# Optimization experiments

Measured on AMD Instinct MI355X. Metric: run time of the kernel, lower is better.

Reference implementation:

```python
import jax, jax.numpy as jnp
import numpy as np

N_SAMPLES = 512
N_SKIP = 10      # __init__ N: number of skipped steps between kept samples
BURNIN = 100


def _perm_weight(bigram, start, end, p):
    # bigram[p[:-1], p[1:]].sum() + start[p[0]] + end[p[-1]]
    return bigram[p[:-1], p[1:]].sum() + start[p[0]] + end[p[-1]]


def setup_inputs() -> dict:
    key = jax.random.key(0)
    k1, k2, k3 = jax.random.split(key, 3)
    n_words = 4096
    return {
        "n_words": n_words,
        "bigram": jax.random.normal(k1, (n_words, n_words), dtype=jnp.float32),
        "start": jax.random.normal(k2, (n_words,), dtype=jnp.float32),
        "end": jax.random.normal(k3, (n_words,), dtype=jnp.float32),
    }


def reference(n_words, bigram, start, end):
    # Total chain length: burn-in, then one kept sample every (N_SKIP+1) steps.
    T = BURNIN + (N_SAMPLES - 1) * (N_SKIP + 1) + 1
    key = jax.random.key(42)
    kinit, kchain = jax.random.split(key)

    permut0 = jax.random.permutation(kinit, n_words).astype(jnp.int32)
    w0 = _perm_weight(bigram, start, end, permut0)
    idx = jnp.arange(n_words, dtype=jnp.int32)

    def step(carry, k):
        permut, w = carry
        kl, ka, kr, ku = jax.random.split(k, 4)
        # segment length l in [1, n_words-1], start a in [0, n_words-l]
        l = jax.random.randint(kl, (), 1, n_words)
        a = jax.random.randint(ka, (), 0, n_words - l + 1)
        b = a + l
        r = jax.random.randint(kr, (), 0, n_words - l)  # [0, n_words-l-1]
        c = (b + r + 1) % (n_words + 1)
        # The 2-opt block move is a cyclic rotation of one contiguous span:
        #   a < c : rotate span [a, c) left-shifting the block [a,b) after [b,c)
        #   a >= c: rotate span [c, b) moving block [a,b) before [c,a)
        lo = jnp.where(a < c, a, c).astype(jnp.int32)
        hi = jnp.where(a < c, c, b).astype(jnp.int32)
        shift = jnp.where(a < c, b - a, a - c).astype(jnp.int32)
        span = hi - lo  # always >= 1
        src = jnp.where((idx >= lo) & (idx < hi),
                        lo + (idx - lo + shift) % span,
                        idx)
        permut2 = permut[src]
        w2 = _perm_weight(bigram, start, end, permut2)
        u = jax.random.uniform(ku, ())
        # accept iff min(1, exp(w2-w)) > u  <=>  min(w2-w, 0) > log(u)
        accept = jnp.minimum(w2 - w, jnp.float32(0.0)) > jnp.log(u)
        permut_n = jnp.where(accept, permut2, permut)
        w_n = jnp.where(accept, w2, w)
        return (permut_n, w_n), permut_n

    keys = jax.random.split(kchain, T)
    _, perms = jax.lax.scan(step, (permut0, w0), keys)  # [T, n_words]
    samples = perms[BURNIN::(N_SKIP + 1)][:N_SAMPLES]   # [n_samples, n_words]
    return samples
```

## Files before the change

kernel.cpp:

```cpp
#include <hip/hip_runtime.h>
#include <stdint.h>
#include <math.h>

#define NW      4096
#define TSTEPS  5722
#define BURN    100
#define SSTRIDE 11
#define NTHR    256
#define NBOUND  522

struct K2 { uint32_t a, b; };

__device__ __forceinline__ K2 tf(uint32_t k0, uint32_t k1, uint32_t c0, uint32_t c1) {
  uint32_t ks2 = k0 ^ k1 ^ 0x1BD11BDAu;
  uint32_t x0 = c0 + k0, x1 = c1 + k1;
#define RR(r) { x0 += x1; x1 = (x1 << (r)) | (x1 >> (32 - (r))); x1 ^= x0; }
  RR(13) RR(15) RR(26) RR(6)
  x0 += k1;  x1 += ks2 + 1u;
  RR(17) RR(29) RR(16) RR(24)
  x0 += ks2; x1 += k0 + 2u;
  RR(13) RR(15) RR(26) RR(6)
  x0 += k0;  x1 += k1 + 3u;
  RR(17) RR(29) RR(16) RR(24)
  x0 += k1;  x1 += ks2 + 4u;
  RR(13) RR(15) RR(26) RR(6)
  x0 += ks2; x1 += k0 + 5u;
#undef RR
  K2 r; r.a = x0; r.b = x1; return r;
}

__device__ __forceinline__ uint32_t xbits(K2 k) {
  K2 r = tf(k.a, k.b, 0u, 0u);
  return r.a ^ r.b;
}

__device__ __forceinline__ uint32_t ri_off(K2 key, uint32_t span) {
  K2 k1 = tf(key.a, key.b, 0u, 0u);
  K2 k2 = tf(key.a, key.b, 0u, 1u);
  uint32_t hb = xbits(k1);
  uint32_t lb = xbits(k2);
  uint32_t m = 65536u % span;
  m = (m * m) % span;
  return ((hb % span) * m + (lb % span)) % span;
}

__device__ __noinline__ void make_prop(uint32_t kca, uint32_t kcb, int t,
                                       uint32_t& lohi, uint32_t& shv, float& lg) {
  K2 kt = tf(kca, kcb, 0u, (uint32_t)t);
  K2 kl = tf(kt.a, kt.b, 0u, 0u);
  K2 ka = tf(kt.a, kt.b, 0u, 1u);
  K2 kr = tf(kt.a, kt.b, 0u, 2u);
  K2 ku = tf(kt.a, kt.b, 0u, 3u);
  uint32_t l = 1u + ri_off(kl, 4095u);
  uint32_t a = ri_off(ka, 4097u - l);
  uint32_t b = a + l;
  uint32_t r = ri_off(kr, 4096u - l);
  uint32_t c = (b + r + 1u) % 4097u;
  uint32_t lo, hi, sh;
  if (a < c) { lo = a; hi = c; sh = b - a; }
  else       { lo = c; hi = b; sh = a - c; }
  uint32_t ub = xbits(ku);
  float uf = __uint_as_float((ub >> 9) | 0x3F800000u) - 1.0f;
  lohi = lo | (hi << 16);
  shv  = sh;
  lg   = (float)log((double)uf);
}

__device__ __forceinline__ uint32_t smap2(uint32_t i, uint32_t lo, uint32_t span, uint32_t sh) {
  uint32_t t = i - lo;
  uint32_t u = t + sh;
  u = (u >= span) ? u - span : u;
  return (t < span) ? lo + u : i;
}

__global__ void prop_kernel(uint4* __restrict__ gprop) {
  int t = blockIdx.x * 256 + threadIdx.x;
  if (t >= TSTEPS) return;
  K2 kchain = tf(0u, 42u, 0u, 1u);
  uint32_t lohi, shv; float lg;
  make_prop(kchain.a, kchain.b, t, lohi, shv, lg);
  gprop[t] = make_uint4(lohi, shv, __float_as_uint(lg), 0u);
}

#define SYNC() do { asm volatile("s_waitcnt lgkmcnt(0)" ::: "memory"); \
                    __builtin_amdgcn_s_barrier(); } while (0)

template<int CTRL>
__device__ __forceinline__ double dpp_f64(double v) {
  long long s = __double_as_longlong(v);
  int lo = (int)(s & 0xFFFFFFFFll);
  int hi = (int)(s >> 32);
  lo = __builtin_amdgcn_update_dpp(0, lo, CTRL, 0xF, 0xF, true);
  hi = __builtin_amdgcn_update_dpp(0, hi, CTRL, 0xF, 0xF, true);
  return __longlong_as_double((long long)(unsigned)lo | ((long long)hi << 32));
}

__device__ __forceinline__ uint32_t compose_sw(uint32_t pos, int jc,
                                               const uint32_t (&mlh)[12],
                                               const uint32_t (&msh)[12]) {
  switch (jc) {
    case 11: pos = smap2(pos, mlh[10] & 0xFFFFu, mlh[10] >> 16, msh[10]); [[fallthrough]];
    case 10: pos = smap2(pos, mlh[9]  & 0xFFFFu, mlh[9]  >> 16, msh[9]);  [[fallthrough]];
    case 9:  pos = smap2(pos, mlh[8]  & 0xFFFFu, mlh[8]  >> 16, msh[8]);  [[fallthrough]];
    case 8:  pos = smap2(pos, mlh[7]  & 0xFFFFu, mlh[7]  >> 16, msh[7]);  [[fallthrough]];
    case 7:  pos = smap2(pos, mlh[6]  & 0xFFFFu, mlh[6]  >> 16, msh[6]);  [[fallthrough]];
    case 6:  pos = smap2(pos, mlh[5]  & 0xFFFFu, mlh[5]  >> 16, msh[5]);  [[fallthrough]];
    case 5:  pos = smap2(pos, mlh[4]  & 0xFFFFu, mlh[4]  >> 16, msh[4]);  [[fallthrough]];
    case 4:  pos = smap2(pos, mlh[3]  & 0xFFFFu, mlh[3]  >> 16, msh[3]);  [[fallthrough]];
    case 3:  pos = smap2(pos, mlh[2]  & 0xFFFFu, mlh[2]  >> 16, msh[2]);  [[fallthrough]];
    case 2:  pos = smap2(pos, mlh[1]  & 0xFFFFu, mlh[1]  >> 16, msh[1]);  [[fallthrough]];
    case 1:  pos = smap2(pos, mlh[0]  & 0xFFFFu, mlh[0]  >> 16, msh[0]);  break;
    default: break;
  }
  return pos;
}

__device__ __forceinline__ void mat_emit(int tid, int jcu, uint32_t cur,
                                         const uint32_t* __restrict__ s_mvlh,
                                         const uint32_t* __restrict__ s_mvsh,
                                         uint32_t (*s_base)[NW],
                                         bool emit, int row, int* __restrict__ out) {
  uint32_t posa[16];
  #pragma unroll
  for (int k = 0; k < 16; ++k) posa[k] = (uint32_t)tid + (uint32_t)k * 256u;
  for (int j = jcu - 1; j >= 0; --j) {
    uint32_t lh = s_mvlh[j], sh = s_mvsh[j];
    uint32_t lo = lh & 0xFFFFu, sp = lh >> 16;
    #pragma unroll
    for (int k = 0; k < 16; ++k) posa[k] = smap2(posa[k], lo, sp, sh);
  }
  uint32_t vals[16];
  #pragma unroll
  for (int k = 0; k < 16; ++k) vals[k] = s_base[cur][posa[k]];
  #pragma unroll
  for (int k = 0; k < 16; ++k) {
    uint32_t i = (uint32_t)tid + (uint32_t)k * 256u;
    s_base[cur ^ 1u][i] = vals[k];
    if (emit) out[(size_t)row * NW + i] = (int)vals[k];
  }
}

__device__ __forceinline__ void stepf(
    int T, uint32_t lane, float sgn, float& ld, bool& accp, int& jc,
    uint32_t (&mlh)[12], uint32_t (&msh)[12],
    uint32_t& s0lh, uint32_t& s0sh, float& s0lg,
    uint32_t& s1lh, uint32_t& s1sh, float& s1lg,
    uint32_t& s2lh, uint32_t& s2sh, float& s2lg,
    uint32_t& s3lh, uint32_t& s3sh, float& s3lg,
    const uint32_t* __restrict__ sbase,
    uint32_t* __restrict__ s_mvlh, uint32_t* __restrict__ s_mvsh,
    const float* __restrict__ bigram, const float* __restrict__ startw,
    const float* __restrict__ endw, const uint4* __restrict__ gprop,
    uint32_t kca, uint32_t kcb) {

  uint32_t p    = lane & 7u;
  uint32_t vset = (lane >> 3) & 3u;

  uint32_t lo2 = s2lh & 0xFFFFu, hi2 = s2lh >> 16, sh2 = s2sh;
  uint32_t g0 = lo2, g1 = lo2 + sh2, g2v = g1 - 1u, g3 = hi2 - 1u;
  uint32_t g4 = (lo2 > 0u) ? lo2 - 1u : 0u;
  uint32_t g5 = (hi2 < (uint32_t)NW) ? hi2 : 0u;
  uint32_t pos = (p == 0u) ? g0 : (p == 1u) ? g1 : (p == 2u) ? g2v
               : (p == 3u) ? g3 : (p == 4u) ? g4 : g5;

  uint32_t lo1 = s1lh & 0xFFFFu, sp1 = (s1lh >> 16) - lo1, sh1 = s1sh;
  uint32_t lo0 = s0lh & 0xFFFFu, sp0 = (s0lh >> 16) - lo0, sh0 = s0sh;
  if (vset & 1u) pos = smap2(pos, lo1, sp1, sh1);
  if (vset & 2u) pos = smap2(pos, lo0, sp0, sh0);
  pos = compose_sw(pos, jc, mlh, msh);
  uint32_t val = sbase[pos];

  int tq = T + 4; if (tq > TSTEPS - 1) tq = TSTEPS - 1;
  uint32_t nlh, nsh; float nlg;
  if (gprop) { uint4 gp = gprop[tq]; nlh = gp.x; nsh = gp.y; nlg = __uint_as_float(gp.z); }
  else       { make_prop(kca, kcb, tq, nlh, nsh, nlg); }

  double du = (double)(ld * sgn);
  du += dpp_f64<0x111>(du);
  du += dpp_f64<0x112>(du);
  du += dpp_f64<0x114>(du);
  double dmin = du < 0.0 ? du : 0.0;
  int accl = (dmin > (double)s0lg) ? 1 : 0;
  int accR = __builtin_amdgcn_readlane(accl, 7);
  int accA = __builtin_amdgcn_readlane(accl, 15);
  int acc = accp ? accA : accR;

  uint32_t qv = (uint32_t)__shfl((int)val, (int)((uint32_t)acc * 16u + lane), 64);
  uint32_t base8 = lane & ~7u;
  uint32_t rsrc = (p == 0u) ? 3u : (p == 1u) ? 2u : (p <= 3u) ? 4u : (p == 4u) ? 2u : 3u;
  uint32_t csrc = (p == 0u) ? 0u : (p <= 2u) ? 1u : (p == 3u) ? 0u : 5u;
  uint32_t row = (uint32_t)__shfl((int)qv, (int)(base8 + rsrc), 64);
  uint32_t col = (uint32_t)__shfl((int)qv, (int)(base8 + csrc), 64);
  bool isbi = (p < 2u) || ((p < 4u) ? (lo2 > 0u) : (hi2 < (uint32_t)NW));
  const float* addr = isbi ? (bigram + (size_t)row * NW + col)
                           : ((p < 4u) ? (startw + col) : (endw + row));
  bool isload = (vset < 2u) && (p < 6u);
  if (isload) ld = *addr;

  if (acc) {
    uint32_t nv = lo0 | (sp0 << 16);
    switch (jc) {
      case 0:  mlh[0]  = nv; msh[0]  = sh0; break;
      case 1:  mlh[1]  = nv; msh[1]  = sh0; break;
      case 2:  mlh[2]  = nv; msh[2]  = sh0; break;
      case 3:  mlh[3]  = nv; msh[3]  = sh0; break;
      case 4:  mlh[4]  = nv; msh[4]  = sh0; break;
      case 5:  mlh[5]  = nv; msh[5]  = sh0; break;
      case 6:  mlh[6]  = nv; msh[6]  = sh0; break;
      case 7:  mlh[7]  = nv; msh[7]  = sh0; break;
      case 8:  mlh[8]  = nv; msh[8]  = sh0; break;
      case 9:  mlh[9]  = nv; msh[9]  = sh0; break;
      case 10: mlh[10] = nv; msh[10] = sh0; break;
      default: break;
    }
    if (lane == 0u) { s_mvlh[jc] = nv; s_mvsh[jc] = sh0; }
    jc++;
  }
  accp = (acc != 0);

  s0lh = s1lh; s0sh = s1sh; s0lg = s1lg;
  s1lh = s2lh; s1sh = s2sh; s1lg = s2lg;
  s2lh = s3lh; s2sh = s3sh; s2lg = s3lg;
  s3lh = nlh;  s3sh = nsh;  s3lg = nlg;
}

__global__ __launch_bounds__(NTHR)
void TwoOptMCMC_86148454023515_kernel(const float* __restrict__ bigram,
                                      const float* __restrict__ startw,
                                      const float* __restrict__ endw,
                                      int* __restrict__ out,
                                      const uint4* __restrict__ gprop) {
  __shared__ __align__(16) uint32_t s_base[2][NW];
  __shared__ uint32_t s_mvlh[12];
  __shared__ uint32_t s_mvsh[12];
  __shared__ uint32_t s_jc[1];

  unsigned long long* s_comp = (unsigned long long*)s_base;
  const int tid = threadIdx.x;
  K2 kinit  = tf(0u, 42u, 0u, 0u);
  K2 kchain = tf(0u, 42u, 0u, 1u);

  {
    K2 kc = kinit;
    for (int rnd = 0; rnd < 2; ++rnd) {
      K2 knext = tf(kc.a, kc.b, 0u, 0u);
      K2 ksub  = tf(kc.a, kc.b, 0u, 1u);
      for (int i = tid; i < NW; i += NTHR) {
        K2 r = tf(ksub.a, ksub.b, 0u, (uint32_t)i);
        uint32_t sk = r.a ^ r.b;
        unsigned long long pv = (rnd == 0) ? (unsigned long long)(uint32_t)i
                                           : (s_comp[i] & 0xFFFull);
        s_comp[i] = ((unsigned long long)sk << 24) |
                    ((unsigned long long)(uint32_t)i << 12) | pv;
      }
      __syncthreads();
      for (int k = 2; k <= NW; k <<= 1) {
        for (int j = k >> 1; j > 0; j >>= 1) {
          for (int i = tid; i < NW; i += NTHR) {
            int ixj = i ^ j;
            if (ixj > i) {
              unsigned long long va = s_comp[i], vb = s_comp[ixj];
              bool up = ((i & k) == 0);
              if ((va > vb) == up) { s_comp[i] = vb; s_comp[ixj] = va; }
            }
          }
          __syncthreads();
        }
      }
      kc = knext;
    }
    uint32_t pv[16];
    #pragma unroll
    for (int k = 0; k < 16; ++k) pv[k] = (uint32_t)(s_comp[tid + k * 256] & 0xFFFull);
    __syncthreads();
    #pragma unroll
    for (int k = 0; k < 16; ++k) s_base[0][tid + k * 256] = pv[k];
    __syncthreads();
  }

  const int wave = tid >> 6;
  const uint32_t lane = (uint32_t)(tid & 63);

  if (wave == 0) {
    uint32_t mlh[12], msh[12];
    #pragma unroll
    for (int k = 0; k < 12; ++k) { mlh[k] = 0u; msh[k] = 0u; }
    int jc = 0; bool accp = false; uint32_t cur = 0u;
    float ldA = 0.f, ldB = 0.f;

    uint32_t s0lh, s0sh, s1lh, s1sh, s2lh, s2sh, s3lh, s3sh;
    float s0lg, s1lg, s2lg, s3lg;
    {
      uint32_t lh[4], sh[4]; float lg[4];
      #pragma unroll
      for (int j = 0; j < 4; ++j) {
        int tq = j; if (tq > TSTEPS - 1) tq = TSTEPS - 1;
        if (gprop) { uint4 gp = gprop[tq]; lh[j] = gp.x; sh[j] = gp.y; lg[j] = __uint_as_float(gp.z); }
        else       { make_prop(kchain.a, kchain.b, tq, lh[j], sh[j], lg[j]); }
      }
      s0lh = lh[0]; s0sh = sh[0]; s0lg = lg[0];
      s1lh = lh[1]; s1sh = sh[1]; s1lg = lg[1];
      s2lh = lh[2]; s2sh = sh[2]; s2lg = lg[2];
      s3lh = lh[3]; s3sh = sh[3]; s3lg = lg[3];
    }

    uint32_t p = lane & 7u;
    uint32_t vset = (lane >> 3) & 3u;
    float sgn = (p >= 6u) ? 0.f : ((p & 1u) ? -1.f : 1.f);
    uint32_t rsrc = (p == 0u) ? 3u : (p == 1u) ? 2u : (p <= 3u) ? 4u : (p == 4u) ? 2u : 3u;
    uint32_t csrc = (p == 0u) ? 0u : (p <= 2u) ? 1u : (p == 3u) ? 0u : 5u;
    bool isload = (vset < 2u) && (p < 6u);
    uint32_t base8 = lane & ~7u;

    {
      uint32_t lo2 = s0lh & 0xFFFFu, hi2 = s0lh >> 16, sh2 = s0sh;
      uint32_t g0 = lo2, g1 = lo2 + sh2, g2v = g1 - 1u, g3 = hi2 - 1u;
      uint32_t g4 = (lo2 > 0u) ? lo2 - 1u : 0u;
      uint32_t g5 = (hi2 < (uint32_t)NW) ? hi2 : 0u;
      uint32_t pos = (p == 0u) ? g0 : (p == 1u) ? g1 : (p == 2u) ? g2v
                   : (p == 3u) ? g3 : (p == 4u) ? g4 : g5;
      uint32_t val = s_base[0][pos];
      uint32_t row = (uint32_t)__shfl((int)val, (int)(base8 + rsrc), 64);
      uint32_t col = (uint32_t)__shfl((int)val, (int)(base8 + csrc), 64);
      bool isbi = (p < 2u) || ((p < 4u) ? (lo2 > 0u) : (hi2 < (uint32_t)NW));
      const float* addr = isbi ? (bigram + (size_t)row * NW + col)
                               : ((p < 4u) ? (startw + col) : (endw + row));
      if (isload) ldA = *addr;
    }
    {
      uint32_t lo2 = s1lh & 0xFFFFu, hi2 = s1lh >> 16, sh2 = s1sh;
      uint32_t g0 = lo2, g1 = lo2 + sh2, g2v = g1 - 1u, g3 = hi2 - 1u;
      uint32_t g4 = (lo2 > 0u) ? lo2 - 1u : 0u;
      uint32_t g5 = (hi2 < (uint32_t)NW) ? hi2 : 0u;
      uint32_t pos = (p == 0u) ? g0 : (p == 1u) ? g1 : (p == 2u) ? g2v
                   : (p == 3u) ? g3 : (p == 4u) ? g4 : g5;
      uint32_t lo0 = s0lh & 0xFFFFu, sp0 = (s0lh >> 16) - lo0, sh0 = s0sh;
      if (vset & 1u) pos = smap2(pos, lo0, sp0, sh0);
      uint32_t val = s_base[0][pos];
      uint32_t row = (uint32_t)__shfl((int)val, (int)(base8 + rsrc), 64);
      uint32_t col = (uint32_t)__shfl((int)val, (int)(base8 + csrc), 64);
      bool isbi = (p < 2u) || ((p < 4u) ? (lo2 > 0u) : (hi2 < (uint32_t)NW));
      const float* addr = isbi ? (bigram + (size_t)row * NW + col)
                               : ((p < 4u) ? (startw + col) : (endw + row));
      if (isload) ldB = *addr;
    }

    int t = 0;
    for (int b = 0; b < NBOUND; ++b) {
      int wlen = (b < 10) ? 10 : ((b == 10) ? 1 : 11);
      const uint32_t* sb = s_base[cur];
      #pragma unroll
      for (int k = 0; k < 11; ++k) {
        if (k < wlen) {
          if ((k & 1) == 0)
            stepf(t + k, lane, sgn, ldA, accp, jc, mlh, msh,
                  s0lh, s0sh, s0lg, s1lh, s1sh, s1lg, s2lh, s2sh, s2lg,
                  s3lh, s3sh, s3lg, sb, s_mvlh, s_mvsh,
                  bigram, startw, endw, gprop, kchain.a, kchain.b);
          else
            stepf(t + k, lane, sgn, ldB, accp, jc, mlh, msh,
                  s0lh, s0sh, s0lg, s1lh, s1sh, s1lg, s2lh, s2sh, s2lg,
                  s3lh, s3sh, s3lg, sb, s_mvlh, s_mvsh,
                  bigram, startw, endw, gprop, kchain.a, kchain.b);
        }
      }
      if (lane == 0u) s_jc[0] = (uint32_t)jc;
      SYNC();
      mat_emit(tid, jc, cur, s_mvlh, s_mvsh, s_base, b >= 10, b - 10, out);
      SYNC();
      if (wlen & 1) { float tmp = ldA; ldA = ldB; ldB = tmp; }
      jc = 0; cur ^= 1u; t += wlen;
    }
  } else {
    for (int b = 0; b < NBOUND; ++b) {
      SYNC();
      int jcu = __builtin_amdgcn_readfirstlane((int)s_jc[0]);
      mat_emit(tid, jcu, (uint32_t)(b & 1), s_mvlh, s_mvsh, s_base, b >= 10, b - 10, out);
      SYNC();
    }
  }
}

extern "C" void kernel_launch(void* const* d_in, const int* in_sizes, int n_in,
                              void* d_out, int out_size, void* d_ws, size_t ws_size,
                              hipStream_t stream) {
  (void)in_sizes; (void)n_in; (void)out_size;
  const float* bigram = (const float*)d_in[1];
  const float* startw = (const float*)d_in[2];
  const float* endw   = (const float*)d_in[3];
  int* out = (int*)d_out;
  uint4* gprop = nullptr;
  if (ws_size >= (size_t)TSTEPS * 16) {
    gprop = (uint4*)d_ws;
    hipLaunchKernelGGL(prop_kernel, dim3((TSTEPS + 255) / 256), dim3(256), 0, stream, gprop);
  }
  hipLaunchKernelGGL(TwoOptMCMC_86148454023515_kernel, dim3(1), dim3(NTHR), 0, stream,
                     bigram, startw, endw, out, gprop);
}
```

Before: 5.516 ms.

## Batch proposal generation per block across lanes and broadcast via readlane

Each proposal used to be generated or loaded per step inside the serial step function, with a software shift register of proposal state. Now each block of up to 11 steps has its proposals produced in parallel, one per lane (14 lanes), prefetched one block ahead. Each step pulls them out with compile-time readlane. The accept-select shuffle is also folded into the row/col shuffles, removing one cross-lane shuffle from the serial critical path. The cost is more scalar readlane traffic and a live vector of next-block proposals.

```diff
diff --git a/kernel.cpp b/kernel.cpp
--- a/kernel.cpp
+++ b/kernel.cpp
@@ -140,21 +140,28 @@
   }
 }
 
+template<int K>
 __device__ __forceinline__ void stepf(
-    int T, uint32_t lane, float sgn, float& ld, bool& accp, int& jc,
+    uint32_t lane, float sgn, float& ld, bool& accp, int& jc,
     uint32_t (&mlh)[12], uint32_t (&msh)[12],
-    uint32_t& s0lh, uint32_t& s0sh, float& s0lg,
-    uint32_t& s1lh, uint32_t& s1sh, float& s1lg,
-    uint32_t& s2lh, uint32_t& s2sh, float& s2lg,
-    uint32_t& s3lh, uint32_t& s3sh, float& s3lg,
+    uint32_t cAlh, uint32_t cAsh, float cAlg,
     const uint32_t* __restrict__ sbase,
     uint32_t* __restrict__ s_mvlh, uint32_t* __restrict__ s_mvsh,
     const float* __restrict__ bigram, const float* __restrict__ startw,
-    const float* __restrict__ endw, const uint4* __restrict__ gprop,
-    uint32_t kca, uint32_t kcb) {
-
-  uint32_t p    = lane & 7u;
+    const float* __restrict__ endw,
+    uint32_t rsrc, uint32_t csrc, bool isload, uint32_t base8) {
+
+  uint32_t p = lane & 7u;
   uint32_t vset = (lane >> 3) & 3u;
+
+  uint32_t s0lh = (uint32_t)__builtin_amdgcn_readlane((int)cAlh, K);
+  uint32_t s0sh = (uint32_t)__builtin_amdgcn_readlane((int)cAsh, K);
+  float    s0lg = __uint_as_float((uint32_t)__builtin_amdgcn_readlane(
+                      (int)__float_as_uint(cAlg), K));
+  uint32_t s1lh = (uint32_t)__builtin_amdgcn_readlane((int)cAlh, K + 1);
+  uint32_t s1sh = (uint32_t)__builtin_amdgcn_readlane((int)cAsh, K + 1);
+  uint32_t s2lh = (uint32_t)__builtin_amdgcn_readlane((int)cAlh, K + 2);
+  uint32_t s2sh = (uint32_t)__builtin_amdgcn_readlane((int)cAsh, K + 2);
 
   uint32_t lo2 = s2lh & 0xFFFFu, hi2 = s2lh >> 16, sh2 = s2sh;
   uint32_t g0 = lo2, g1 = lo2 + sh2, g2v = g1 - 1u, g3 = hi2 - 1u;
@@ -169,11 +176,6 @@
   if (vset & 2u) pos = smap2(pos, lo0, sp0, sh0);
   pos = compose_sw(pos, jc, mlh, msh);
   uint32_t val = sbase[pos];
-
-  int tq = T + 4; if (tq > TSTEPS - 1) tq = TSTEPS - 1;
-  uint32_t nlh, nsh; float nlg;
-  if (gprop) { uint4 gp = gprop[tq]; nlh = gp.x; nsh = gp.y; nlg = __uint_as_float(gp.z); }
-  else       { make_prop(kca, kcb, tq, nlh, nsh, nlg); }
 
   double du = (double)(ld * sgn);
   du += dpp_f64<0x111>(du);
@@ -185,16 +187,12 @@
   int accA = __builtin_amdgcn_readlane(accl, 15);
   int acc = accp ? accA : accR;
 
-  uint32_t qv = (uint32_t)__shfl((int)val, (int)((uint32_t)acc * 16u + lane), 64);
-  uint32_t base8 = lane & ~7u;
-  uint32_t rsrc = (p == 0u) ? 3u : (p == 1u) ? 2u : (p <= 3u) ? 4u : (p == 4u) ? 2u : 3u;
-  uint32_t csrc = (p == 0u) ? 0u : (p <= 2u) ? 1u : (p == 3u) ? 0u : 5u;
-  uint32_t row = (uint32_t)__shfl((int)qv, (int)(base8 + rsrc), 64);
-  uint32_t col = (uint32_t)__shfl((int)qv, (int)(base8 + csrc), 64);
+  uint32_t selb = (uint32_t)acc * 16u + base8;
+  uint32_t row = (uint32_t)__shfl((int)val, (int)(selb + rsrc), 64);
+  uint32_t col = (uint32_t)__shfl((int)val, (int)(selb + csrc), 64);
   bool isbi = (p < 2u) || ((p < 4u) ? (lo2 > 0u) : (hi2 < (uint32_t)NW));
   const float* addr = isbi ? (bigram + (size_t)row * NW + col)
                            : ((p < 4u) ? (startw + col) : (endw + row));
-  bool isload = (vset < 2u) && (p < 6u);
   if (isload) ld = *addr;
 
   if (acc) {
@@ -217,11 +215,6 @@
     jc++;
   }
   accp = (acc != 0);
-
-  s0lh = s1lh; s0sh = s1sh; s0lg = s1lg;
-  s1lh = s2lh; s1sh = s2sh; s1lg = s2lg;
-  s2lh = s3lh; s2sh = s3sh; s2lg = s3lg;
-  s3lh = nlh;  s3sh = nsh;  s3lg = nlg;
 }
 
 __global__ __launch_bounds__(NTHR)
@@ -288,22 +281,6 @@
     int jc = 0; bool accp = false; uint32_t cur = 0u;
     float ldA = 0.f, ldB = 0.f;
 
-    uint32_t s0lh, s0sh, s1lh, s1sh, s2lh, s2sh, s3lh, s3sh;
-    float s0lg, s1lg, s2lg, s3lg;
-    {
-      uint32_t lh[4], sh[4]; float lg[4];
-      #pragma unroll
-      for (int j = 0; j < 4; ++j) {
-        int tq = j; if (tq > TSTEPS - 1) tq = TSTEPS - 1;
-        if (gprop) { uint4 gp = gprop[tq]; lh[j] = gp.x; sh[j] = gp.y; lg[j] = __uint_as_float(gp.z); }
-        else       { make_prop(kchain.a, kchain.b, tq, lh[j], sh[j], lg[j]); }
-      }
-      s0lh = lh[0]; s0sh = sh[0]; s0lg = lg[0];
-      s1lh = lh[1]; s1sh = sh[1]; s1lg = lg[1];
-      s2lh = lh[2]; s2sh = sh[2]; s2lg = lg[2];
-      s3lh = lh[3]; s3sh = sh[3]; s3lg = lg[3];
-    }
-
     uint32_t p = lane & 7u;
     uint32_t vset = (lane >> 3) & 3u;
     float sgn = (p >= 6u) ? 0.f : ((p & 1u) ? -1.f : 1.f);
@@ -312,7 +289,16 @@
     bool isload = (vset < 2u) && (p < 6u);
     uint32_t base8 = lane & ~7u;
 
+    uint32_t cAlh, cAsh; float cAlg;
     {
+      int idx = (int)(lane < 14u ? lane : 13u);
+      if (gprop) { uint4 gp = gprop[idx]; cAlh = gp.x; cAsh = gp.y; cAlg = __uint_as_float(gp.z); }
+      else       { make_prop(kchain.a, kchain.b, idx, cAlh, cAsh, cAlg); }
+    }
+
+    {
+      uint32_t s0lh = (uint32_t)__builtin_amdgcn_readlane((int)cAlh, 0);
+      uint32_t s0sh = (uint32_t)__builtin_amdgcn_readlane((int)cAsh, 0);
       uint32_t lo2 = s0lh & 0xFFFFu, hi2 = s0lh >> 16, sh2 = s0sh;
       uint32_t g0 = lo2, g1 = lo2 + sh2, g2v = g1 - 1u, g3 = hi2 - 1u;
       uint32_t g4 = (lo2 > 0u) ? lo2 - 1u : 0u;
@@ -328,6 +314,10 @@
       if (isload) ldA = *addr;
     }
     {
+      uint32_t s0lh = (uint32_t)__builtin_amdgcn_readlane((int)cAlh, 0);
+      uint32_t s0sh = (uint32_t)__builtin_amdgcn_readlane((int)cAsh, 0);
+      uint32_t s1lh = (uint32_t)__builtin_amdgcn_readlane((int)cAlh, 1);
+      uint32_t s1sh = (uint32_t)__builtin_amdgcn_readlane((int)cAsh, 1);
       uint32_t lo2 = s1lh & 0xFFFFu, hi2 = s1lh >> 16, sh2 = s1sh;
       uint32_t g0 = lo2, g1 = lo2 + sh2, g2v = g1 - 1u, g3 = hi2 - 1u;
       uint32_t g4 = (lo2 > 0u) ? lo2 - 1u : 0u;
@@ -345,32 +335,40 @@
       if (isload) ldB = *addr;
     }
 
+#define STEPK(K, LD) stepf<K>(lane, sgn, LD, accp, jc, mlh, msh, cAlh, cAsh, cAlg, \
+                              sb, s_mvlh, s_mvsh, bigram, startw, endw,            \
+                              rsrc, csrc, isload, base8)
+
     int t = 0;
     for (int b = 0; b < NBOUND; ++b) {
       int wlen = (b < 10) ? 10 : ((b == 10) ? 1 : 11);
+      int t_next = t + wlen;
+
+      uint32_t nlh, nsh; float nlg;
+      {
+        int idx = t_next + (int)(lane < 14u ? lane : 13u);
+        if (idx > TSTEPS - 1) idx = TSTEPS - 1;
+        if (gprop) { uint4 gp = gprop[idx]; nlh = gp.x; nsh = gp.y; nlg = __uint_as_float(gp.z); }
+        else       { make_prop(kchain.a, kchain.b, idx, nlh, nsh, nlg); }
+      }
+
       const uint32_t* sb = s_base[cur];
-      #pragma unroll
-      for (int k = 0; k < 11; ++k) {
-        if (k < wlen) {
-          if ((k & 1) == 0)
-            stepf(t + k, lane, sgn, ldA, accp, jc, mlh, msh,
-                  s0lh, s0sh, s0lg, s1lh, s1sh, s1lg, s2lh, s2sh, s2lg,
-                  s3lh, s3sh, s3lg, sb, s_mvlh, s_mvsh,
-                  bigram, startw, endw, gprop, kchain.a, kchain.b);
-          else
-            stepf(t + k, lane, sgn, ldB, accp, jc, mlh, msh,
-                  s0lh, s0sh, s0lg, s1lh, s1sh, s1lg, s2lh, s2sh, s2lg,
-                  s3lh, s3sh, s3lg, sb, s_mvlh, s_mvsh,
-                  bigram, startw, endw, gprop, kchain.a, kchain.b);
-        }
+      STEPK(0, ldA);
+      if (wlen > 1) {
+        STEPK(1, ldB); STEPK(2, ldA); STEPK(3, ldB); STEPK(4, ldA);
+        STEPK(5, ldB); STEPK(6, ldA); STEPK(7, ldB); STEPK(8, ldA); STEPK(9, ldB);
       }
+      if (wlen > 10) { STEPK(10, ldA); }
+
       if (lane == 0u) s_jc[0] = (uint32_t)jc;
       SYNC();
       mat_emit(tid, jc, cur, s_mvlh, s_mvsh, s_base, b >= 10, b - 10, out);
       SYNC();
       if (wlen & 1) { float tmp = ldA; ldA = ldB; ldB = tmp; }
-      jc = 0; cur ^= 1u; t += wlen;
-    }
+      cAlh = nlh; cAsh = nsh; cAlg = nlg;
+      jc = 0; cur ^= 1u; t = t_next;
+    }
+#undef STEPK
   } else {
     for (int b = 0; b < NBOUND; ++b) {
       SYNC();
```

After: 4.605 ms, median of 2. -16.5%, faster.
